# Kernel optimization log

Measured on AMD Instinct MI355X. Metric: run time of the kernel, lower is better.

## Reference

```python
import jax, jax.numpy as jnp
import numpy as np

N_NODES = 50000
N_EDGES = 800000
IN_DIM = 128
OUT_DIM = 64
HEADS = 8
HEAD_DIM = OUT_DIM // HEADS
NEG_SLOPE = 0.2


def setup_inputs() -> dict:
    key = jax.random.key(0)
    k1, k2, k3, k4, k5 = jax.random.split(key, 5)
    x = jax.random.normal(k1, (N_NODES, IN_DIM), dtype=jnp.float32)
    edge_indices = jax.random.randint(k2, (2, N_EDGES), 0, N_NODES, dtype=jnp.int64)
    # Linear(input_dim, output_dim, bias=False): weight is [out, in]
    W = jax.random.normal(k3, (OUT_DIM, IN_DIM), dtype=jnp.float32) * (1.0 / np.sqrt(IN_DIM))
    src_attn = jax.random.normal(k4, (HEADS, HEAD_DIM), dtype=jnp.float32) * (1.0 / np.sqrt(HEAD_DIM))
    dst_attn = jax.random.normal(k5, (HEADS, HEAD_DIM), dtype=jnp.float32) * (1.0 / np.sqrt(HEAD_DIM))
    return {"x": x, "edge_indices": edge_indices, "W": W, "src_attn": src_attn, "dst_attn": dst_attn}


def reference(x, edge_indices, W, src_attn, dst_attn):
    # Eval mode: all dropouts are identity.
    N = x.shape[0]
    # add self loops
    loops = jnp.arange(N, dtype=edge_indices.dtype)
    ei = jnp.concatenate([edge_indices, jnp.stack([loops, loops])], axis=1)  # [2, E+N]
    row, col = ei[0], ei[1]

    h = (x @ W.T).reshape(N, HEADS, HEAD_DIM)  # [N, H, D]
    s = jnp.einsum("nhd,hd->nh", h, src_attn)  # [N, H]
    d = jnp.einsum("nhd,hd->nh", h, dst_attn)  # [N, H]

    e = jax.nn.leaky_relu(s[row] + d[col], negative_slope=NEG_SLOPE)  # [E', H]

    # segment softmax over rows (torch.sparse.softmax with dim=1 normalizes per row)
    m = jax.ops.segment_max(e, row, num_segments=N)          # [N, H]
    ex = jnp.exp(e - m[row])                                 # [E', H]
    denom = jax.ops.segment_sum(ex, row, num_segments=N)    # [N, H]
    w = ex / denom[row]                                      # [E', H]

    # sparse.mm per head: out[row] += w * h[col]
    msg = w[:, :, None] * h[col]                             # [E', H, D]
    out = jax.ops.segment_sum(msg, row, num_segments=N)      # [N, H, D]
    return out.reshape(N, HEADS * HEAD_DIM)
```

## Files before the change

kernel.cpp:

```cpp
#include <hip/hip_runtime.h>

#define NN 50000
#define NEG_SLOPE 0.2f
#define LOG2E 1.44269504088896340736f

#define GEMM_NB ((NN + 63) / 64)
#define NBUCK3 782
#define EPB 4096
#define CAPQ 1536

typedef __bf16 bf16x8 __attribute__((ext_vector_type(8)));
typedef float f32x4 __attribute__((ext_vector_type(4)));

static __device__ __forceinline__ unsigned short f2bf(float f) {
    __bf16 b = (__bf16)f;
    return __builtin_bit_cast(unsigned short, b);
}
static __device__ __forceinline__ float bf2f(unsigned short u) {
    return __uint_as_float(((unsigned)u) << 16);
}

static __device__ __forceinline__ int detect_i64(const int* __restrict__ ei,
                                                 int lane) {
    unsigned long long b = __ballot(ei[2 * lane + 1] != 0);
    return (b == 0ull) ? 1 : 0;
}

__global__ __launch_bounds__(256) void k_fused0(
        const float* __restrict__ x, const float* __restrict__ W,
        const float* __restrict__ sa, const float* __restrict__ da,
        const int* __restrict__ ei,
        unsigned short* __restrict__ hb, float* __restrict__ s,
        float* __restrict__ d, int* __restrict__ S, int* __restrict__ LP,
        unsigned* __restrict__ tmp, int E, int NB1) {
    __shared__ int hist[1024];
    __shared__ int pref[256];
    __shared__ unsigned lrec[EPB];
    const int tid  = threadIdx.x;
    const int lane = tid & 63;

    if (blockIdx.x >= GEMM_NB) {
        const int bx = blockIdx.x - GEMM_NB;
        hist[tid] = 0; hist[tid + 256] = 0; hist[tid + 512] = 0; hist[tid + 768] = 0;
        const int f = detect_i64(ei, lane);
        __syncthreads();

        const int base = bx * EPB + tid * 16;
        int rw[16], cl[16];
        const bool fullvec = (base + 16 <= E) && ((E & 3) == 0);
        if (f) {
            if (fullvec) {
                const int4* p = (const int4*)(ei + 2 * base);
                const int4* q = (const int4*)(ei + 2 * E + 2 * base);
                #pragma unroll
                for (int g = 0; g < 8; ++g) {
                    int4 a = p[g]; int4 b = q[g];
                    rw[2 * g] = a.x; rw[2 * g + 1] = a.z;
                    cl[2 * g] = b.x; cl[2 * g + 1] = b.z;
                }
            } else {
                #pragma unroll
                for (int k = 0; k < 16; ++k) {
                    int e = base + k;
                    rw[k] = (e < E) ? ei[2 * e] : -1;
                    cl[k] = (e < E) ? ei[2 * E + 2 * e] : 0;
                }
            }
        } else {
            if (fullvec) {
                const int4* p = (const int4*)(ei + base);
                const int4* q = (const int4*)(ei + E + base);
                #pragma unroll
                for (int g = 0; g < 4; ++g) {
                    int4 a = p[g]; int4 b = q[g];
                    rw[4 * g] = a.x; rw[4 * g + 1] = a.y;
                    rw[4 * g + 2] = a.z; rw[4 * g + 3] = a.w;
                    cl[4 * g] = b.x; cl[4 * g + 1] = b.y;
                    cl[4 * g + 2] = b.z; cl[4 * g + 3] = b.w;
                }
            } else {
                #pragma unroll
                for (int k = 0; k < 16; ++k) {
                    int e = base + k;
                    rw[k] = (e < E) ? ei[e] : -1;
                    cl[k] = (e < E) ? ei[E + e] : 0;
                }
            }
        }

        #pragma unroll
        for (int k = 0; k < 16; ++k)
            if (rw[k] >= 0) atomicAdd(&hist[rw[k] >> 6], 1);
        __syncthreads();

        const int c0 = hist[4 * tid],     c1 = hist[4 * tid + 1];
        const int c2 = hist[4 * tid + 2], c3 = hist[4 * tid + 3];
        const int tsum = c0 + c1 + c2 + c3;
        pref[tid] = tsum;
        __syncthreads();
        for (int off = 1; off < 256; off <<= 1) {
            int u = (tid >= off) ? pref[tid - off] : 0;
            __syncthreads();
            pref[tid] += u;
            __syncthreads();
        }
        const int e0 = pref[tid] - tsum;
        const int e1 = e0 + c0, e2 = e1 + c1, e3 = e2 + c2;
        const int b0 = 4 * tid;
        if (b0 < NBUCK3)     { S[(b0    ) * NB1 + bx] = c0; LP[(b0    ) * NB1 + bx] = e0; }
        if (b0 + 1 < NBUCK3) { S[(b0 + 1) * NB1 + bx] = c1; LP[(b0 + 1) * NB1 + bx] = e1; }
        if (b0 + 2 < NBUCK3) { S[(b0 + 2) * NB1 + bx] = c2; LP[(b0 + 2) * NB1 + bx] = e2; }
        if (b0 + 3 < NBUCK3) { S[(b0 + 3) * NB1 + bx] = c3; LP[(b0 + 3) * NB1 + bx] = e3; }
        hist[b0] = e0; hist[b0 + 1] = e1; hist[b0 + 2] = e2; hist[b0 + 3] = e3;
        __syncthreads();

        #pragma unroll
        for (int k = 0; k < 16; ++k) {
            if (rw[k] >= 0) {
                int lp = atomicAdd(&hist[rw[k] >> 6], 1);
                lrec[lp] = ((unsigned)rw[k] << 16) | (unsigned)cl[k];
            }
        }
        __syncthreads();

        const int tot = pref[255];
        for (int j = tid; j < tot; j += 256) {
            const unsigned v = lrec[j];
            tmp[bx * EPB + j] = (((v >> 16) & 63u) << 24) | (v & 0xFFFFu);
        }
        return;
    }

    const int wave = tid >> 6;
    const int c    = lane & 15;
    const int kg   = lane >> 4;
    const int n0   = blockIdx.x * 64 + wave * 16;

    bf16x8 bf[4][4];
    #pragma unroll
    for (int kt = 0; kt < 4; ++kt) {
        #pragma unroll
        for (int ot = 0; ot < 4; ++ot) {
            const float* wp = &W[(ot * 16 + c) * 128 + kt * 32 + kg * 8];
            f32x4 w0 = *(const f32x4*)wp;
            f32x4 w1 = *(const f32x4*)(wp + 4);
            bf16x8 b;
            #pragma unroll
            for (int j = 0; j < 4; ++j) { b[j] = (__bf16)w0[j]; b[4 + j] = (__bf16)w1[j]; }
            bf[kt][ot] = b;
        }
    }

    int nr = n0 + c; if (nr > NN - 1) nr = NN - 1;
    const float* xp = &x[(long)nr * 128 + kg * 8];

    f32x4 acc[4] = {};
    #pragma unroll
    for (int kt = 0; kt < 4; ++kt) {
        f32x4 x0 = *(const f32x4*)(xp + kt * 32);
        f32x4 x1 = *(const f32x4*)(xp + kt * 32 + 4);
        bf16x8 a;
        #pragma unroll
        for (int j = 0; j < 4; ++j) { a[j] = (__bf16)x0[j]; a[4 + j] = (__bf16)x1[j]; }
        #pragma unroll
        for (int ot = 0; ot < 4; ++ot)
            acc[ot] = __builtin_amdgcn_mfma_f32_16x16x32_bf16(a, bf[kt][ot], acc[ot], 0, 0, 0);
    }

    float sav[4], dav[4];
    #pragma unroll
    for (int ot = 0; ot < 4; ++ot) {
        sav[ot] = sa[ot * 16 + c] * LOG2E;
        dav[ot] = da[ot * 16 + c] * LOG2E;
    }

    const int nodebase = n0 + kg * 4;
    #pragma unroll
    for (int r = 0; r < 4; ++r) {
        const int n = nodebase + r;
        const bool ok = (n < NN);
        if (ok) {
            #pragma unroll
            for (int ot = 0; ot < 4; ++ot) hb[n * 64 + ot * 16 + c] = f2bf(acc[ot][r]);
        }
        float ps[4], pd[4];
        #pragma unroll
        for (int ot = 0; ot < 4; ++ot) { ps[ot] = acc[ot][r] * sav[ot]; pd[ot] = acc[ot][r] * dav[ot]; }
        #pragma unroll
        for (int m = 1; m < 8; m <<= 1) {
            #pragma unroll
            for (int ot = 0; ot < 4; ++ot) {
                ps[ot] += __shfl_xor(ps[ot], m, 64);
                pd[ot] += __shfl_xor(pd[ot], m, 64);
            }
        }
        if (ok && (c & 7) == 0) {
            const int hbid = c >> 3;
            #pragma unroll
            for (int ot = 0; ot < 4; ++ot) {
                s[n * 8 + 2 * ot + hbid] = ps[ot];
                d[n * 8 + 2 * ot + hbid] = pd[ot];
            }
        }
    }
}

__global__ __launch_bounds__(512) void k_bgather(
        const unsigned* __restrict__ tmp, const int* __restrict__ S,
        const int* __restrict__ LP, const unsigned short* __restrict__ hb,
        const float* __restrict__ sarr, const float* __restrict__ d,
        float* __restrict__ out, int NB1) {
    __shared__ int aux2[256];
    __shared__ int aux3[256];
    __shared__ int bins[64];
    __shared__ int pref2[64];
    __shared__ unsigned u_raw[CAPQ];
    __shared__ int lcol[CAPQ];

    const int t    = threadIdx.x;
    const int bkt  = blockIdx.x;
    const int lane = t & 63;
    const int wid  = t >> 6;

    if (t < 256) {
        aux2[t] = (t < NB1) ? S[bkt * NB1 + t] : 0;
        aux3[t] = (t < NB1) ? LP[bkt * NB1 + t] : 0;
    }
    if (t >= 256 && t < 320) bins[t - 256] = 0;
    __syncthreads();
    for (int off = 1; off < 256; off <<= 1) {
        int u = 0;
        if (t < 256 && t >= off) u = aux2[t - off];
        __syncthreads();
        if (t < 256) aux2[t] += u;
        __syncthreads();
    }
    int cnt = aux2[255]; if (cnt > CAPQ) cnt = CAPQ;

    for (int p = t; p < cnt; p += 512) {
        int lo = 0, hi = 255;
        #pragma unroll
        for (int it = 0; it < 8; ++it) {
            const int mid = (lo + hi) >> 1;
            if (aux2[mid] > p) hi = mid; else lo = mid + 1;
        }
        const int excl = lo ? aux2[lo - 1] : 0;
        const unsigned v = tmp[lo * EPB + aux3[lo] + (p - excl)];
        u_raw[p] = v;
        atomicAdd(&bins[v >> 24], 1);
    }
    __syncthreads();

    const int bv = (t < 64) ? bins[t] : 0;
    if (t < 64) pref2[t] = bv;
    __syncthreads();
    for (int off = 1; off < 64; off <<= 1) {
        int u = 0;
        if (t < 64 && t >= off) u = pref2[t - off];
        __syncthreads();
        if (t < 64) pref2[t] += u;
        __syncthreads();
    }
    if (t < 64) bins[t] = pref2[t] - bv;
    __syncthreads();
    for (int i = t; i < cnt; i += 512) {
        const unsigned v = u_raw[i];
        const int p = atomicAdd(&bins[v >> 24], 1);
        lcol[p] = (int)(v & 0xFFFFu);
    }
    __syncthreads();

    const int o    = lane;
    const int oh   = o >> 3;
    const int eidx = lane >> 3;
    const int h    = lane & 7;

    #pragma unroll
    for (int j = 0; j < 8; ++j) {
        const int rl = j * 8 + wid;
        const int n  = bkt * 64 + rl;
        if (n >= NN) continue;

        const int bgn = rl ? pref2[rl - 1] : 0;
        const int end = pref2[rl];

        const float sn_h = sarr[n * 8 + h];
        float acc  = 0.0f;
        float dsum = 0.0f;

        for (int i = bgn; i < end; i += 8) {
            const int myi  = i + eidx;
            const bool val = (myi < end);
            const int c = lcol[val ? myi : (end - 1)];
            float dv = d[c * 8 + h];
            float v = sn_h + dv;
            v = fmaxf(v, NEG_SLOPE * v);
            v = val ? v : -10000.0f;
            const float ev = __builtin_amdgcn_exp2f(v);
            dsum += ev;

            #pragma unroll
            for (int k = 0; k < 8; ++k) {
                const int   c_k = __builtin_amdgcn_readlane(c, k * 8);
                const float e_k = __shfl(ev, k * 8 + oh);
                acc += e_k * bf2f(hb[c_k * 64 + o]);
            }
        }

        dsum += __shfl_xor(dsum, 8, 64);
        dsum += __shfl_xor(dsum, 16, 64);
        dsum += __shfl_xor(dsum, 32, 64);
        float denom = __shfl(dsum, oh);

        const float sn_o = sarr[n * 8 + oh];
        const float dn_o = d[n * 8 + oh];
        float vs = sn_o + dn_o;
        vs = fmaxf(vs, NEG_SLOPE * vs);
        const float es = __builtin_amdgcn_exp2f(vs);
        denom += es;
        acc += es * bf2f(hb[n * 64 + o]);

        out[n * 64 + o] = acc / denom;
    }
}

extern "C" void kernel_launch(void* const* d_in, const int* in_sizes, int n_in,
                              void* d_out, int out_size, void* d_ws, size_t ws_size,
                              hipStream_t stream) {
    const float* x  = (const float*)d_in[0];
    const int*   ei = (const int*)d_in[1];
    const float* W  = (const float*)d_in[2];
    const float* sa = (const float*)d_in[3];
    const float* da = (const float*)d_in[4];
    float* out = (float*)d_out;
    const int E = in_sizes[1] / 2;

    int NB1 = (E + EPB - 1) / EPB;
    if (NB1 > 256) NB1 = 256;

    unsigned short* hb = (unsigned short*)d_ws;
    float* s  = (float*)(hb + NN * 64);
    float* dd = s + NN * 8;
    int* S    = (int*)(dd + NN * 8);
    int* LP   = S + NBUCK3 * 256;
    unsigned* tmp = (unsigned*)(LP + NBUCK3 * 256);

    k_fused0<<<GEMM_NB + NB1, 256, 0, stream>>>(x, W, sa, da, ei,
                                                hb, s, dd, S, LP, tmp, E, NB1);
    k_bgather<<<NBUCK3, 512, 0, stream>>>(tmp, S, LP, hb, s, dd, out, NB1);
}
```

Measured before the change: 68.31 us.

## Precompute per-edge attention weights into LDS before the gather loop

Adds a block-wide pass that computes exp2(leaky_relu(s+d)) for every bucketed edge and stores it as bf16 in shared memory. Source scores are staged in LDS. The per-row gather loop then reads the column indices with vector LDS loads and the weights directly, replacing the per-iteration shuffles, readlanes and the final cross-lane denominator reduction. The cost is more LDS, an extra barrier, and bf16 rounding of the attention weights. The vector index loads may read unaligned or uninitialised tail entries; those are masked only through a zero weight, while the gather address still uses them.

```diff
diff --git a/kernel.cpp b/kernel.cpp
--- a/kernel.cpp
+++ b/kernel.cpp
@@ -215,7 +215,9 @@
     __shared__ int bins[64];
     __shared__ int pref2[64];
     __shared__ unsigned u_raw[CAPQ];
-    __shared__ int lcol[CAPQ];
+    __shared__ unsigned lcol[CAPQ + 8];
+    __shared__ float s_lds[512];
+    __shared__ unsigned short P[(CAPQ + 8) * 8];
 
     const int t    = threadIdx.x;
     const int bkt  = blockIdx.x;
@@ -227,6 +229,11 @@
         aux3[t] = (t < NB1) ? LP[bkt * NB1 + t] : 0;
     }
     if (t >= 256 && t < 320) bins[t - 256] = 0;
+    {
+        int n = bkt * 64 + (t >> 3);
+        if (n > NN - 1) n = NN - 1;
+        s_lds[t] = sarr[n * 8 + (t & 7)];
+    }
     __syncthreads();
     for (int off = 1; off < 256; off <<= 1) {
         int u = 0;
@@ -266,14 +273,26 @@
     for (int i = t; i < cnt; i += 512) {
         const unsigned v = u_raw[i];
         const int p = atomicAdd(&bins[v >> 24], 1);
-        lcol[p] = (int)(v & 0xFFFFu);
-    }
-    __syncthreads();
-
-    const int o    = lane;
-    const int oh   = o >> 3;
-    const int eidx = lane >> 3;
-    const int h    = lane & 7;
+        lcol[p] = v;
+    }
+    __syncthreads();
+
+    const int h8 = t & 7;
+    for (int e0 = 0; e0 < cnt; e0 += 64) {
+        const int e = e0 + (t >> 3);
+        if (e < cnt) {
+            const unsigned rec = lcol[e];
+            const int c  = (int)(rec & 0xFFFFu);
+            const int r6 = (int)(rec >> 24);
+            float v = s_lds[r6 * 8 + h8] + d[c * 8 + h8];
+            v = fmaxf(v, NEG_SLOPE * v);
+            P[e * 8 + h8] = f2bf(__builtin_amdgcn_exp2f(v));
+        }
+    }
+    __syncthreads();
+
+    const int o  = lane;
+    const int oh = o >> 3;
 
     #pragma unroll
     for (int j = 0; j < 8; ++j) {
@@ -284,43 +303,31 @@
         const int bgn = rl ? pref2[rl - 1] : 0;
         const int end = pref2[rl];
 
-        const float sn_h = sarr[n * 8 + h];
         float acc  = 0.0f;
         float dsum = 0.0f;
 
         for (int i = bgn; i < end; i += 8) {
-            const int myi  = i + eidx;
-            const bool val = (myi < end);
-            const int c = lcol[val ? myi : (end - 1)];
-            float dv = d[c * 8 + h];
-            float v = sn_h + dv;
-            v = fmaxf(v, NEG_SLOPE * v);
-            v = val ? v : -10000.0f;
-            const float ev = __builtin_amdgcn_exp2f(v);
-            dsum += ev;
-
+            const uint4 ca = *(const uint4*)&lcol[i];
+            const uint4 cb = *(const uint4*)&lcol[i + 4];
+            const unsigned cs[8] = { ca.x & 0xFFFFu, ca.y & 0xFFFFu,
+                                     ca.z & 0xFFFFu, ca.w & 0xFFFFu,
+                                     cb.x & 0xFFFFu, cb.y & 0xFFFFu,
+                                     cb.z & 0xFFFFu, cb.w & 0xFFFFu };
             #pragma unroll
             for (int k = 0; k < 8; ++k) {
-                const int   c_k = __builtin_amdgcn_readlane(c, k * 8);
-                const float e_k = __shfl(ev, k * 8 + oh);
-                acc += e_k * bf2f(hb[c_k * 64 + o]);
-            }
-        }
-
-        dsum += __shfl_xor(dsum, 8, 64);
-        dsum += __shfl_xor(dsum, 16, 64);
-        dsum += __shfl_xor(dsum, 32, 64);
-        float denom = __shfl(dsum, oh);
-
-        const float sn_o = sarr[n * 8 + oh];
+                const unsigned short pu = P[(i + k) * 8 + oh];
+                const float e_k = (i + k < end) ? bf2f(pu) : 0.0f;
+                dsum += e_k;
+                acc  += e_k * bf2f(hb[cs[k] * 64 + o]);
+            }
+        }
+
+        const float sn_o = s_lds[rl * 8 + oh];
         const float dn_o = d[n * 8 + oh];
         float vs = sn_o + dn_o;
         vs = fmaxf(vs, NEG_SLOPE * vs);
         const float es = __builtin_amdgcn_exp2f(vs);
-        denom += es;
-        acc += es * bf2f(hb[n * 64 + o]);
-
-        out[n * 64 + o] = acc / denom;
+        out[n * 64 + o] = (acc + es * bf2f(hb[n * 64 + o])) / (dsum + es);
     }
 }
 
```

After: 89.60 us. 1.31x slower.
